# Optimization experiments

Measured on AMD Instinct MI355X. Metric: run time of the kernel, lower is better.

The kernel has to match this reference:

```python
import jax, jax.numpy as jnp
import numpy as np

L, B, D, N = 4096, 8, 1024, 16


def setup_inputs() -> dict:
    key = jax.random.key(0)
    ks = jax.random.split(key, 6)
    # ema_expansion_matrix init: alternating +-1 plus small noise (per reset_parameters)
    sign = jnp.where(jnp.arange(N) % 2 == 1, -1.0, 1.0)[None, :, None]
    return {
        "x": jax.random.normal(ks[0], (L, B, D), dtype=jnp.float32),
        "damping_factor": 0.2 * jax.random.normal(ks[1], (D, N, 1), dtype=jnp.float32),
        "decay_factor": 0.2 * jax.random.normal(ks[2], (D, N, 1), dtype=jnp.float32),
        "ema_expansion_matrix": sign + 0.02 * jax.random.normal(ks[3], (D, N, 1), dtype=jnp.float32),
        "kernel_projection_matrix": jax.random.normal(ks[4], (D, N), dtype=jnp.float32),
        "residual_weight": jax.random.normal(ks[5], (D,), dtype=jnp.float32),
    }


def reference(x, damping_factor, decay_factor, ema_expansion_matrix,
              kernel_projection_matrix, residual_weight):
    # x: (L, B, D)
    length = x.shape[0]
    num_heads = damping_factor.shape[1]
    scaling = (1.0 / num_heads) ** 0.5

    residual = x * residual_weight  # (L, B, D)
    xc = jnp.transpose(x, (1, 2, 0))  # (B, D, L)

    # EMA coefficients
    p = jax.nn.sigmoid(damping_factor)                     # (D, N, 1)
    q = 1.0 - p * jax.nn.sigmoid(decay_factor)             # (D, N, 1)

    # Vandermonde kernel: (D, N, L) -> project to (D, L)
    t = jnp.arange(length, dtype=x.dtype)[None, None, :]
    kernel_dnl = p * ema_expansion_matrix * jnp.exp(t * jnp.log(q))
    kernel = jnp.einsum('dnl,dn->dl', kernel_dnl, kernel_projection_matrix * scaling)

    # Causal FFT convolution with n = 2L
    n_fft = 2 * length
    k_f = jnp.fft.rfft(kernel, n=n_fft)                    # (D, n/2+1)
    x_f = jnp.fft.rfft(xc, n=n_fft)                        # (B, D, n/2+1)
    out = jnp.fft.irfft(x_f * k_f, n=n_fft)[..., :length]  # (B, D, L)

    out = jnp.transpose(out, (2, 0, 1)) + residual         # (L, B, D)
    return jax.nn.relu(out)
```

## Files before the change

### kernel.cpp

```cpp
#include <hip/hip_runtime.h>
#include <math.h>

#define L 4096
#define B 8
#define D 1024
#define NH 16
#define COUT 128
#define WB 128
#define NCHUNK (L / COUT)
#define BD 8192

#define REP16(F) F(0) F(1) F(2) F(3) F(4) F(5) F(6) F(7) F(8) F(9) F(10) F(11) F(12) F(13) F(14) F(15)
#define REP8(F)  F(0) F(1) F(2) F(3) F(4) F(5) F(6) F(7)

__device__ __forceinline__ float sigmoidf(float v) {
    return 1.0f / (1.0f + __expf(-v));
}

#define UPD(i) s##i = fmaf(q##i, s##i, xv);
#define UPDALL UPD(0) UPD(1) UPD(2) UPD(3) UPD(4) UPD(5) UPD(6) UPD(7)
#define ACC(i) s##i = fmaf(q##i, s##i, xv); y = fmaf(P##i, s##i, y);
#define ACCALL ACC(0) ACC(1) ACC(2) ACC(3) ACC(4) ACC(5) ACC(6) ACC(7)

__global__ void __launch_bounds__(256, 8)
ema_fused(const float* __restrict__ x,
          const float* __restrict__ damp,
          const float* __restrict__ decay,
          const float* __restrict__ ema,
          const float* __restrict__ proj,
          const float* __restrict__ rw,
          float* __restrict__ out) {
    const int tid  = threadIdx.x;
    const int lane = tid & 63;
    const int wv   = tid >> 6;
    const int h    = lane & 1;
    const int dl   = lane >> 1;
    const int d    = blockIdx.x * 128 + wv * 32 + dl;
    const int c    = blockIdx.y;
    const int b    = blockIdx.z;

    const float* dp = damp  + d * NH + h * 8;
    const float* dc = decay + d * NH + h * 8;
    const float* de = ema   + d * NH + h * 8;
    const float* pj = proj  + d * NH + h * 8;

#define DECLQS(i) float q##i, s##i;
    REP8(DECLQS)
#define INITQS(i) { q##i = 1.0f - sigmoidf(dp[i]) * sigmoidf(dc[i]); s##i = 0.0f; }
    REP8(INITQS)

    const size_t base = (size_t)b * D + d;

    if (c > 0) {
        const float* xp = x + (size_t)(c * COUT - WB) * BD + base;
#define LDA16(i) float a##i = xp[i * BD];
        REP16(LDA16)
        xp += 16 * BD;
        for (int r = 0; r < WB - 16; r += 16) {
#define LDB16(i) float t##i = xp[i * BD];
            REP16(LDB16)
            xp += 16 * BD;
#define CONS16(i) { float xv = a##i; UPDALL }
            REP16(CONS16)
#define MOV16(i) a##i = t##i;
            REP16(MOV16)
        }
        REP16(CONS16)
    }

#define DECLP(i) float P##i;
    REP8(DECLP)
#define INITP(i) { float p_ = sigmoidf(dp[i]); P##i = p_ * de[i] * pj[i] * 0.25f; }
    REP8(INITP)
    const float weff = (h == 0) ? rw[d] : 0.0f;

    const float* xp = x   + (size_t)(c * COUT) * BD + base;
    float*       op = out + (size_t)(c * COUT) * BD + base;

#define EMIT(v, k) { float xv = (v); float y = xv * weff; ACCALL \
                     y += __shfl_xor(y, 1); \
                     if (h == 0) __builtin_nontemporal_store(fmaxf(y, 0.0f), op + (k) * BD); }

#define LDA8(i) float a##i = xp[i * BD];
    REP8(LDA8)
    xp += 8 * BD;
    for (int r = 0; r < COUT - 8; r += 8) {
#define LDB8(i) float t##i = xp[i * BD];
        REP8(LDB8)
        xp += 8 * BD;
#define EM8(i) EMIT(a##i, i)
        REP8(EM8)
        op += 8 * BD;
#define MOV8(i) a##i = t##i;
        REP8(MOV8)
    }
    REP8(EM8)
}

extern "C" void kernel_launch(void* const* d_in, const int* in_sizes, int n_in,
                              void* d_out, int out_size, void* d_ws, size_t ws_size,
                              hipStream_t stream) {
    const float* x     = (const float*)d_in[0];
    const float* damp  = (const float*)d_in[1];
    const float* decay = (const float*)d_in[2];
    const float* ema   = (const float*)d_in[3];
    const float* proj  = (const float*)d_in[4];
    const float* rw    = (const float*)d_in[5];
    float* out = (float*)d_out;

    dim3 grid(D / 128, NCHUNK, B);
    ema_fused<<<grid, 256, 0, stream>>>(x, damp, decay, ema, proj, rw, out);
}
```

Before: 307.3 us.

## Stage x tiles into LDS via async global_load_lds double buffering

Replaces per-thread register prefetching of x with a double-buffered LDS pipeline. The block cooperatively issues 16-byte global_load_lds copies of 16-row tiles while it computes on the previous tile. Warmup and output phases now share one loop. The aim is wide coalesced loads that overlap with the recurrence, at the cost of a block-wide barrier per tile and LDS occupancy that may limit how many blocks fit per CU.

```diff
diff --git a/kernel.cpp b/kernel.cpp
--- a/kernel.cpp
+++ b/kernel.cpp
@@ -9,8 +9,9 @@
 #define WB 128
 #define NCHUNK (L / COUT)
 #define BD 8192
+#define DBLK 128
+#define TL 16
 
-#define REP16(F) F(0) F(1) F(2) F(3) F(4) F(5) F(6) F(7) F(8) F(9) F(10) F(11) F(12) F(13) F(14) F(15)
 #define REP8(F)  F(0) F(1) F(2) F(3) F(4) F(5) F(6) F(7)
 
 __device__ __forceinline__ float sigmoidf(float v) {
@@ -21,6 +22,10 @@
 #define UPDALL UPD(0) UPD(1) UPD(2) UPD(3) UPD(4) UPD(5) UPD(6) UPD(7)
 #define ACC(i) s##i = fmaf(q##i, s##i, xv); y = fmaf(P##i, s##i, y);
 #define ACCALL ACC(0) ACC(1) ACC(2) ACC(3) ACC(4) ACC(5) ACC(6) ACC(7)
+
+#define GLD16(g, l) __builtin_amdgcn_global_load_lds( \
+    (const __attribute__((address_space(1))) unsigned int*)(g), \
+    (__attribute__((address_space(3))) unsigned int*)(l), 16, 0, 0)
 
 __global__ void __launch_bounds__(256, 8)
 ema_fused(const float* __restrict__ x,
@@ -34,10 +39,13 @@
     const int lane = tid & 63;
     const int wv   = tid >> 6;
     const int h    = lane & 1;
-    const int dl   = lane >> 1;
-    const int d    = blockIdx.x * 128 + wv * 32 + dl;
+    const int dloc = (wv << 5) + (lane >> 1);
+    const int d0   = blockIdx.x * DBLK;
+    const int d    = d0 + dloc;
     const int c    = blockIdx.y;
     const int b    = blockIdx.z;
+
+    __shared__ float lds[2][TL * DBLK];
 
     const float* dp = damp  + d * NH + h * 8;
     const float* dc = decay + d * NH + h * 8;
@@ -48,53 +56,59 @@
     REP8(DECLQS)
 #define INITQS(i) { q##i = 1.0f - sigmoidf(dp[i]) * sigmoidf(dc[i]); s##i = 0.0f; }
     REP8(INITQS)
-
-    const size_t base = (size_t)b * D + d;
-
-    if (c > 0) {
-        const float* xp = x + (size_t)(c * COUT - WB) * BD + base;
-#define LDA16(i) float a##i = xp[i * BD];
-        REP16(LDA16)
-        xp += 16 * BD;
-        for (int r = 0; r < WB - 16; r += 16) {
-#define LDB16(i) float t##i = xp[i * BD];
-            REP16(LDB16)
-            xp += 16 * BD;
-#define CONS16(i) { float xv = a##i; UPDALL }
-            REP16(CONS16)
-#define MOV16(i) a##i = t##i;
-            REP16(MOV16)
-        }
-        REP16(CONS16)
-    }
-
 #define DECLP(i) float P##i;
     REP8(DECLP)
 #define INITP(i) { float p_ = sigmoidf(dp[i]); P##i = p_ * de[i] * pj[i] * 0.25f; }
     REP8(INITP)
     const float weff = (h == 0) ? rw[d] : 0.0f;
 
-    const float* xp = x   + (size_t)(c * COUT) * BD + base;
-    float*       op = out + (size_t)(c * COUT) * BD + base;
+    const int nt = (c > 0) ? (WB + COUT) / TL : COUT / TL;
+    const int wt = (c > 0) ? WB / TL : 0;
 
-#define EMIT(v, k) { float xv = (v); float y = xv * weff; ACCALL \
-                     y += __shfl_xor(y, 1); \
-                     if (h == 0) __builtin_nontemporal_store(fmaxf(y, 0.0f), op + (k) * BD); }
+    const float* xb = x + (size_t)(c * COUT - (c > 0 ? WB : 0)) * BD
+                        + (size_t)b * D + d0;
 
-#define LDA8(i) float a##i = xp[i * BD];
-    REP8(LDA8)
-    xp += 8 * BD;
-    for (int r = 0; r < COUT - 8; r += 8) {
-#define LDB8(i) float t##i = xp[i * BD];
-        REP8(LDB8)
-        xp += 8 * BD;
-#define EM8(i) EMIT(a##i, i)
-        REP8(EM8)
-        op += 8 * BD;
-#define MOV8(i) a##i = t##i;
-        REP8(MOV8)
+    const int scol = (lane & 31) << 2;
+    const int srow = (wv << 2) + (lane >> 5);
+
+    {
+        const float* g0 = xb + (size_t)srow * BD + scol;
+        float* l0 = &lds[0][(wv << 2) * DBLK];
+        GLD16(g0, l0);
+        GLD16(g0 + (size_t)2 * BD, l0 + 2 * DBLK);
     }
-    REP8(EM8)
+    __syncthreads();
+
+    float* opb = out + (size_t)(c * COUT) * BD + (size_t)b * D + d;
+
+    for (int t = 0; t < nt; ++t) {
+        if (t + 1 < nt) {
+            const float* g0 = xb + (size_t)((t + 1) * TL + srow) * BD + scol;
+            float* l0 = &lds[(t + 1) & 1][(wv << 2) * DBLK];
+            GLD16(g0, l0);
+            GLD16(g0 + (size_t)2 * BD, l0 + 2 * DBLK);
+        }
+        const float* buf = lds[t & 1];
+        if (t < wt) {
+#pragma unroll
+            for (int sl = 0; sl < TL; ++sl) {
+                float xv = buf[sl * DBLK + dloc];
+                UPDALL
+            }
+        } else {
+            float* op = opb + (size_t)(t - wt) * TL * BD;
+#pragma unroll
+            for (int sl = 0; sl < TL; ++sl) {
+                float xv = buf[sl * DBLK + dloc];
+                float y = xv * weff;
+                ACCALL
+                y += __shfl_xor(y, 1);
+                if (h == 0)
+                    __builtin_nontemporal_store(fmaxf(y, 0.0f), op + (size_t)sl * BD);
+            }
+        }
+        __syncthreads();
+    }
 }
 
 extern "C" void kernel_launch(void* const* d_in, const int* in_sizes, int n_in,
@@ -108,6 +122,6 @@
     const float* rw    = (const float*)d_in[5];
     float* out = (float*)d_out;
 
-    dim3 grid(D / 128, NCHUNK, B);
+    dim3 grid(D / DBLK, NCHUNK, B);
     ema_fused<<<grid, 256, 0, stream>>>(x, damp, decay, ema, proj, rw, out);
 }
```

New measurement: 283.2 us. 7.8% less time.

## Stream x tiles through LDS with async global_load_lds multi-buffering

Applied to the files above, without the earlier changes.

Replaces per-thread strided register loads of x with wave-level 16-byte global_load_lds transfers into a four-slot LDS ring buffer, using hand-placed vmcnt waits to keep several tiles in flight during warmup and output phases. The aim is wider, coalesced loads and overlap of memory latency with the recurrence compute. It relies on manual vmcnt accounting that must account for the nontemporal stores, which risks subtle ordering bugs, and it adds LDS usage that could affect occupancy.

```diff
diff --git a/kernel.cpp b/kernel.cpp
--- a/kernel.cpp
+++ b/kernel.cpp
@@ -9,8 +9,10 @@
 #define WB 128
 #define NCHUNK (L / COUT)
 #define BD 8192
+#define DBLK 128
+#define TL 8
+#define NBUF 4
 
-#define REP16(F) F(0) F(1) F(2) F(3) F(4) F(5) F(6) F(7) F(8) F(9) F(10) F(11) F(12) F(13) F(14) F(15)
 #define REP8(F)  F(0) F(1) F(2) F(3) F(4) F(5) F(6) F(7)
 
 __device__ __forceinline__ float sigmoidf(float v) {
@@ -21,6 +23,13 @@
 #define UPDALL UPD(0) UPD(1) UPD(2) UPD(3) UPD(4) UPD(5) UPD(6) UPD(7)
 #define ACC(i) s##i = fmaf(q##i, s##i, xv); y = fmaf(P##i, s##i, y);
 #define ACCALL ACC(0) ACC(1) ACC(2) ACC(3) ACC(4) ACC(5) ACC(6) ACC(7)
+
+#define GLD16(g, l) __builtin_amdgcn_global_load_lds( \
+    (const __attribute__((address_space(1))) unsigned int*)(g), \
+    (__attribute__((address_space(3))) unsigned int*)(l), 16, 0, 0)
+
+#define VM(n) asm volatile("s_waitcnt vmcnt(" #n ")" ::: "memory")
+#define MEMFENCE asm volatile("" ::: "memory")
 
 __global__ void __launch_bounds__(256, 8)
 ema_fused(const float* __restrict__ x,
@@ -35,9 +44,12 @@
     const int wv   = tid >> 6;
     const int h    = lane & 1;
     const int dl   = lane >> 1;
-    const int d    = blockIdx.x * 128 + wv * 32 + dl;
+    const int dloc = (wv << 5) + dl;
+    const int d    = blockIdx.x * DBLK + dloc;
     const int c    = blockIdx.y;
     const int b    = blockIdx.z;
+
+    __shared__ float lds[4][NBUF][TL][32];
 
     const float* dp = damp  + d * NH + h * 8;
     const float* dc = decay + d * NH + h * 8;
@@ -48,53 +60,64 @@
     REP8(DECLQS)
 #define INITQS(i) { q##i = 1.0f - sigmoidf(dp[i]) * sigmoidf(dc[i]); s##i = 0.0f; }
     REP8(INITQS)
-
-    const size_t base = (size_t)b * D + d;
-
-    if (c > 0) {
-        const float* xp = x + (size_t)(c * COUT - WB) * BD + base;
-#define LDA16(i) float a##i = xp[i * BD];
-        REP16(LDA16)
-        xp += 16 * BD;
-        for (int r = 0; r < WB - 16; r += 16) {
-#define LDB16(i) float t##i = xp[i * BD];
-            REP16(LDB16)
-            xp += 16 * BD;
-#define CONS16(i) { float xv = a##i; UPDALL }
-            REP16(CONS16)
-#define MOV16(i) a##i = t##i;
-            REP16(MOV16)
-        }
-        REP16(CONS16)
-    }
-
 #define DECLP(i) float P##i;
     REP8(DECLP)
 #define INITP(i) { float p_ = sigmoidf(dp[i]); P##i = p_ * de[i] * pj[i] * 0.25f; }
     REP8(INITP)
     const float weff = (h == 0) ? rw[d] : 0.0f;
 
-    const float* xp = x   + (size_t)(c * COUT) * BD + base;
-    float*       op = out + (size_t)(c * COUT) * BD + base;
+    const int wb = (c > 0) ? WB : 0;
+    const int wt = wb / TL;
 
-#define EMIT(v, k) { float xv = (v); float y = xv * weff; ACCALL \
-                     y += __shfl_xor(y, 1); \
-                     if (h == 0) __builtin_nontemporal_store(fmaxf(y, 0.0f), op + (k) * BD); }
+    const float* xw = x + (size_t)(c * COUT - wb) * BD + (size_t)b * D
+                        + (size_t)blockIdx.x * DBLK + (wv << 5);
+    const float* gsrc = xw + (size_t)(lane >> 3) * BD + ((lane & 7) << 2);
 
-#define LDA8(i) float a##i = xp[i * BD];
-    REP8(LDA8)
-    xp += 8 * BD;
-    for (int r = 0; r < COUT - 8; r += 8) {
-#define LDB8(i) float t##i = xp[i * BD];
-        REP8(LDB8)
-        xp += 8 * BD;
-#define EM8(i) EMIT(a##i, i)
-        REP8(EM8)
-        op += 8 * BD;
-#define MOV8(i) a##i = t##i;
-        REP8(MOV8)
+#define GLD(t) GLD16(gsrc + (size_t)(t) * (TL * BD), &lds[wv][(t) & 3][0][0])
+
+    GLD(0); GLD(1); GLD(2);
+    MEMFENCE;
+
+    if (c > 0) {
+#pragma unroll 4
+        for (int t = 0; t < WB / TL; ++t) {
+            VM(2);
+            GLD(t + 3);
+            MEMFENCE;
+            const float* bp = &lds[wv][t & 3][0][dl];
+#pragma unroll
+            for (int sl = 0; sl < TL; ++sl) { float xv = bp[sl * 32]; UPDALL }
+        }
     }
-    REP8(EM8)
+
+    float* opb = out + (size_t)(c * COUT) * BD + (size_t)b * D + d;
+
+#define OTILE(r, KWAIT, DOGLD) { \
+        KWAIT; \
+        if (DOGLD) GLD(wt + (r) + 3); \
+        MEMFENCE; \
+        const float* bp = &lds[wv][(r) & 3][0][dl]; \
+        float* op = opb + (size_t)(r) * (TL * BD); \
+        _Pragma("unroll") \
+        for (int sl = 0; sl < TL; ++sl) { \
+            float xv = bp[sl * 32]; \
+            float y = xv * weff; \
+            ACCALL \
+            y += __shfl_xor(y, 1); \
+            if (h == 0) \
+                __builtin_nontemporal_store(fmaxf(y, 0.0f), op + (size_t)sl * BD); \
+        } }
+
+    OTILE(0,  VM(2),  1)
+    OTILE(1,  VM(10), 1)
+    OTILE(2,  VM(18), 1)
+    OTILE(3,  VM(26), 1)
+#pragma unroll 4
+    for (int r = 4; r <= 11; ++r) { OTILE(r, VM(26), 1) }
+    OTILE(12, VM(26), 1)
+    OTILE(13, VM(26), 0)
+    OTILE(14, VM(24), 0)
+    OTILE(15, VM(24), 0)
 }
 
 extern "C" void kernel_launch(void* const* d_in, const int* in_sizes, int n_in,
@@ -108,6 +131,6 @@
     const float* rw    = (const float*)d_in[5];
     float* out = (float*)d_out;
 
-    dim3 grid(D / 128, NCHUNK, B);
+    dim3 grid(D / DBLK, NCHUNK, B);
     ema_fused<<<grid, 256, 0, stream>>>(x, damp, decay, ema, proj, rw, out);
 }
```

Result: no change. 307.3 us (+0.0%).
